# Kernel tuning notes

Hardware: AMD Instinct MI355X
Metric: run time of the kernel (lower is better)

## Reference

```python
import jax, jax.numpy as jnp
import numpy as np

DIM = 100
SAMPLE_DS = 0.5
MAX_S = int(DIM / SAMPLE_DS) + 1  # 201, matches torch sample_ds_arr
DIRECTIONS = ['x', 'x', 'y', 'y']  # constant in the original forward


def _polygon_area(poly):
    # poly: [bs, num_v, 2]; shoelace-style area identical to torch loop
    y_max = jnp.max(poly[:, :, 1], axis=-1)            # [bs]
    x0 = poly[:, :, 0]; y0 = poly[:, :, 1]
    x1 = jnp.roll(x0, -1, axis=1); y1 = jnp.roll(y0, -1, axis=1)
    s = jnp.sum((x1 - x0) * (y_max[:, None] - (y1 + y0) * 0.5), axis=1)
    return jnp.abs(s)


def _line_sum(mask_m, x0, x1, y0, y1, axis_x):
    # mask_m: [bs, DIM, DIM]; x0,x1,y0,y1: [bs, num_v]
    # Vectorized version of torch get_samples + interpolated_sum:
    # masked_select/dedup are replaced by boolean keep masks (samples along an
    # edge are monotone, so the valid set is a contiguous run and "previous
    # compacted sample" == "previous step").
    steps = jnp.arange(MAX_S, dtype=mask_m.dtype)      # [S]
    vx = x1 - x0 + 1e-6
    vy = y1 - y0 + 1e-6
    n = jnp.sqrt(vx * vx + vy * vy)
    vx = vx / n; vy = vy / n
    xs = x0[..., None] + steps * vx[..., None]         # [bs, nv, S]
    ys = y0[..., None] + steps * vy[..., None]
    xlo = jnp.minimum(x0, x1)[..., None]; xhi = jnp.maximum(x0, x1)[..., None]
    ylo = jnp.minimum(y0, y1)[..., None]; yhi = jnp.maximum(y0, y1)[..., None]
    seg = ((xs <= xhi + 1e-3) & (xs >= xlo - 1e-3) &
           (ys <= yhi + 1e-3) & (ys >= ylo - 1e-3))
    u = xs if axis_x else ys
    bound = (u <= DIM - 1) & (u >= 0.0)
    valid = seg & bound
    # dedup on floor(u) along sample axis (torch get_uniques)
    fu = jnp.floor(u)
    prev_valid = jnp.pad(valid[..., :-1], ((0, 0), (0, 0), (1, 0)))
    prev_fu = jnp.pad(fu[..., :-1], ((0, 0), (0, 0), (1, 0)))
    first = valid & ~prev_valid
    keep = valid & (first | (fu != prev_fu))
    # bilinear interpolation (torch interpolated_sum)
    X0f = jnp.floor(xs); Y0f = jnp.floor(ys)
    w00 = (X0f + 1 - xs) * (Y0f + 1 - ys)
    w01 = (X0f + 1 - xs) * (ys - Y0f)
    w10 = (xs - X0f) * (Y0f + 1 - ys)
    w11 = (xs - X0f) * (ys - Y0f)
    Xi0 = jnp.clip(X0f, 0, DIM - 1).astype(jnp.int32)
    Xi1 = jnp.clip(X0f + 1, 0, DIM - 1).astype(jnp.int32)
    Yi0 = jnp.clip(Y0f, 0, DIM - 1).astype(jnp.int32)
    Yi1 = jnp.clip(Y0f + 1, 0, DIM - 1).astype(jnp.int32)
    gather = jax.vmap(lambda m, yy, xx: m[yy, xx])      # over batch
    val = (w00 * gather(mask_m, Yi0, Xi0) + w01 * gather(mask_m, Yi1, Xi0) +
           w10 * gather(mask_m, Yi0, Xi1) + w11 * gather(mask_m, Yi1, Xi1))
    return jnp.sum(jnp.where(keep, val, 0.0), axis=-1)  # [bs, nv]


def _polygon_area_mask(poly, gt_mask):
    # poly: [bs, nv, 2], gt_mask: [bs, 4, DIM, DIM]
    x0 = poly[:, :, 0]; y0 = poly[:, :, 1]
    x1 = jnp.roll(x0, -1, axis=1); y1 = jnp.roll(y0, -1, axis=1)
    ret = jnp.zeros(poly.shape[0], dtype=poly.dtype)
    for m, d in enumerate(DIRECTIONS):
        ax = (d == 'x')
        sign = jnp.where((x1 > x0) if ax else (y1 > y0), 1.0, -1.0)
        sf = _line_sum(gt_mask[:, m], x0, x1, y0, y1, ax)
        sb = _line_sum(gt_mask[:, m], x1, x0, y1, y0, ax)
        s = jnp.sum(sign * (sf + sb) * 0.5, axis=1)
        ret = ret + jnp.abs(s)
    return ret / len(DIRECTIONS)


def setup_inputs() -> dict:
    key = jax.random.key(0)
    k1, k2, k3 = jax.random.split(key, 3)
    bs, nv = 512, 64
    poly = jax.random.uniform(k1, (bs, nv, 2), dtype=jnp.float32) * (DIM - 1)
    gt = jax.random.uniform(k2, (bs, nv, 2), dtype=jnp.float32) * (DIM - 1)
    gt_mask = jax.random.uniform(k3, (bs, 4, DIM, DIM), dtype=jnp.float32)
    return {"poly": poly, "gt": gt, "gt_mask": gt_mask}


def reference(poly, gt, gt_mask):
    pred_area = _polygon_area(poly)
    gt_area = _polygon_area(gt)
    int_area = _polygon_area_mask(poly, gt_mask)
    union_area = pred_area + gt_area - int_area
    return int_area / union_area
```

## Files before the change

### kernel.cpp

```cpp
#include <hip/hip_runtime.h>
#include <math.h>

#define DIM   100
#define NV    64
#define BS    512
#define MAXCH 1664
#define SMW   108
#define SMH   103

template<bool AX>
__device__ __forceinline__ float mainloop(
    const unsigned char* sm, const float4* prmA, const float4* prmB,
    const unsigned short* chunkTab, int totE, int tid) {
  const int grp = tid >> 5;
  const int sub = (tid >> 3) & 3;
  const int st  = tid & 7;
  const int base0 = grp * 16 + sub * 4;
  float acc = 0.0f;

  for (int i = 0; i * 128 < totE; ++i) {
    const ushort4 ent = *reinterpret_cast<const ushort4*>(
        &chunkTab[i * 128 + base0]);

    #define SAMPLE(e) {                                                    \
      const int c = (e) >> 4;                                              \
      const float kf = (float)((((e) & 15) << 3) | st);                    \
      const float4 p = prmA[c];                                            \
      const float4 q = prmB[c];                                            \
      const float vu = AX ? p.z : p.w;                                     \
      const float u0 = AX ? p.x : p.y;                                     \
      const float fu0 = floorf(u0);                                        \
      const float ck = fu0 + __builtin_copysignf(kf, vu);                  \
      const float te = ceilf(fmaf(kf, q.z, q.w));                          \
      const float u1 = __fadd_rn(__fmul_rn(te, vu), u0);                   \
      float t = (floorf(u1) == ck) ? te : (te + 1.0f);                     \
      t = fmaxf(t, 0.0f);                                                  \
      const float xs = __fadd_rn(__fmul_rn(t, p.z), p.x);                  \
      const float ys = __fadd_rn(__fmul_rn(t, p.w), p.y);                  \
      const float X0 = floorf(xs), Y0 = floorf(ys);                        \
      const float wx1 = xs - X0, wy1 = ys - Y0;                            \
      const float wx0 = 1.0f - wx1, wy0 = 1.0f - wy1;                      \
      const int ix = max(min((int)X0, 100), -1);                           \
      const int iy = max(min((int)Y0, 100), -1);                           \
      const int a = iy * SMW + ix;                                         \
      const float g00 = (float)sm[a + (SMW + 4)];                          \
      const float g10 = (float)sm[a + (SMW + 5)];                          \
      const float g01 = (float)sm[a + (2 * SMW + 4)];                      \
      const float g11 = (float)sm[a + (2 * SMW + 5)];                      \
      const float top = fmaf(wx1, g10, wx0 * g00);                         \
      const float bot = fmaf(wx1, g11, wx0 * g01);                         \
      const float val = fmaf(wy1, bot, wy0 * top);                         \
      const float w = (kf <= q.y) ? q.x : 0.0f;                            \
      acc = fmaf(w, val, acc);                                             \
    }
    SAMPLE(ent.x); SAMPLE(ent.y); SAMPLE(ent.z); SAMPLE(ent.w);
    #undef SAMPLE
  }
  return acc;
}

__global__ __launch_bounds__(256, 8) void diffiou_intersect(
    const float* __restrict__ poly, const float* __restrict__ gt_mask,
    float* __restrict__ ws) {
  __shared__ unsigned char sm[SMH * SMW];
  __shared__ float4 prmA[128];
  __shared__ float4 prmB[128];
  __shared__ unsigned short chunkTab[MAXCH];
  __shared__ int   wsum[2];
  __shared__ int   totalChunks;
  __shared__ float red[4];

  const int bid = blockIdx.x;
  const int b   = bid >> 2;
  const int m   = bid & 3;
  const bool ax = (m < 2);
  const int tid = threadIdx.x;

  const float*  src  = gt_mask + (size_t)(b * 4 + m) * (DIM * DIM);
  const float4* src4 = reinterpret_cast<const float4*>(src);

  float4 L0 = src4[tid];
  float4 L1 = src4[tid + 256];
  float4 L2 = src4[tid + 512];
  float4 L3 = src4[tid + 768];
  float4 L4 = src4[tid + 1024];

  #define CVTW(L, j) {                                                     \
    const int r_ = (j) / 25;                                               \
    const int g_ = (j) - r_ * 25;                                          \
    const unsigned int c0 = (unsigned int)__float2int_rn((L).x * 255.0f);  \
    const unsigned int c1 = (unsigned int)__float2int_rn((L).y * 255.0f);  \
    const unsigned int c2 = (unsigned int)__float2int_rn((L).z * 255.0f);  \
    const unsigned int c3 = (unsigned int)__float2int_rn((L).w * 255.0f);  \
    *reinterpret_cast<unsigned int*>(&sm[(r_ + 1) * SMW + 4 + 4 * g_]) =   \
        c0 | (c1 << 8) | (c2 << 16) | (c3 << 24);                          \
  }

  int ncv = 0;
  if (tid < 128) {
    const int e  = tid >> 1;
    const int fb = tid & 1;
    const float* pb = poly + (size_t)b * NV * 2;
    const float ex0 = pb[e * 2 + 0], ey0 = pb[e * 2 + 1];
    const int   en  = (e + 1) & (NV - 1);
    const float ex1 = pb[en * 2 + 0], ey1 = pb[en * 2 + 1];
    const float sign = (ax ? (ex1 > ex0) : (ey1 > ey0)) ? 1.0f : -1.0f;
    const float x0 = fb ? ex1 : ex0, y0 = fb ? ey1 : ey0;
    const float x1 = fb ? ex0 : ex1, y1 = fb ? ey0 : ey1;
    float vx = (x1 - x0) + 1e-6f;
    float vy = (y1 - y0) + 1e-6f;
    const float n = __fsqrt_rn(__fadd_rn(__fmul_rn(vx, vx), __fmul_rn(vy, vy)));
    vx = __fdiv_rn(vx, n);
    vy = __fdiv_rn(vy, n);
    float xlo = fminf(x0, x1) - 0.001f, xhi = fmaxf(x0, x1) + 0.001f;
    float ylo = fminf(y0, y1) - 0.001f, yhi = fmaxf(y0, y1) + 0.001f;
    if (ax) { xlo = fmaxf(xlo, 0.0f); xhi = fminf(xhi, (float)(DIM - 1)); }
    else    { ylo = fmaxf(ylo, 0.0f); yhi = fminf(yhi, (float)(DIM - 1)); }

    #define VALID_AT(tt, out_) {                                  \
      const float tf_ = (float)(tt);                              \
      const float xs_ = __fadd_rn(__fmul_rn(tf_, vx), x0);        \
      const float ys_ = __fadd_rn(__fmul_rn(tf_, vy), y0);        \
      out_ = (xs_ <= xhi) && (xs_ >= xlo) &&                      \
             (ys_ <= yhi) && (ys_ >= ylo);                        \
    }
    int T;
    bool v200; VALID_AT(200, v200);
    if (v200) { T = 200; }
    else {
      int lo = 0, hi = 200;
      #pragma unroll
      for (int it = 0; it < 8; ++it) {
        const int mid = (lo + hi) >> 1;
        bool vm; VALID_AT(mid, vm);
        if (vm) lo = mid; else hi = mid;
      }
      T = lo;
    }
    #undef VALID_AT

    const float vu  = ax ? vx : vy;
    const float u0  = ax ? x0 : y0;
    const float fu0 = floorf(u0);
    const float uT  = __fadd_rn(__fmul_rn((float)T, vu), u0);
    int K = abs((int)floorf(uT) - (int)fu0);
    K = min(K, 99);
    const float B = __fdiv_rn(1.0f, fabsf(vu));
    const float D = (vu > 0.0f) ? (fu0 - u0) : (u0 - fu0 - 1.0f);
    prmA[tid] = make_float4(x0, y0, vx, vy);
    prmB[tid] = make_float4(sign * (0.5f / 255.0f), (float)K,
                            B, fmaf(D, B, -0.005f));
    ncv = (K >> 3) + 1;
  }

  CVTW(L0, tid);
  CVTW(L1, tid + 256);
  CVTW(L2, tid + 512);
  CVTW(L3, tid + 768);
  CVTW(L4, tid + 1024);
  const int j5 = tid + 1280, j6 = tid + 1536, j7 = tid + 1792,
            j8 = tid + 2048, j9 = tid + 2304;
  L0 = src4[j5];
  L1 = src4[j6];
  L2 = src4[j7];
  L3 = src4[j8];
  L4 = (j9 < 2500) ? src4[j9] : make_float4(0.f, 0.f, 0.f, 0.f);

  int v = ncv;
  #pragma unroll
  for (int i = 1; i < 64; i <<= 1) {
    const int w = __shfl_up(v, i, 64);
    if ((tid & 63) >= i) v += w;
  }
  if (((tid & 63) == 63) && (tid < 128)) wsum[tid >> 6] = v;
  __syncthreads();
  if ((tid >= 64) && (tid < 128)) v += wsum[0];
  if (tid < 128) {
    const int start = v - ncv;
    for (int k = 0; k < ncv; ++k)
      chunkTab[start + k] = (unsigned short)((tid << 4) | k);
    if (tid == 127) totalChunks = v;
  }

  CVTW(L0, j5);
  CVTW(L1, j6);
  CVTW(L2, j7);
  CVTW(L3, j8);
  if (j9 < 2500) CVTW(L4, j9);
  if (tid < 75) {
    const int rr = tid / 25;
    const int g  = tid - rr * 25;
    const int srow = (rr == 0) ? 0 : (DIM - 1);
    const int drow = (rr == 0) ? 0 : (100 + rr);
    const float4 q = src4[srow * 25 + g];
    const unsigned int c0 = (unsigned int)__float2int_rn(q.x * 255.0f);
    const unsigned int c1 = (unsigned int)__float2int_rn(q.y * 255.0f);
    const unsigned int c2 = (unsigned int)__float2int_rn(q.z * 255.0f);
    const unsigned int c3 = (unsigned int)__float2int_rn(q.w * 255.0f);
    *reinterpret_cast<unsigned int*>(&sm[drow * SMW + 4 + 4 * g]) =
        c0 | (c1 << 8) | (c2 << 16) | (c3 << 24);
  }
  if (tid < SMH) {
    const int sr = min(max(tid - 1, 0), DIM - 1);
    const unsigned char e0 =
        (unsigned char)__float2int_rn(src[sr * DIM + 0] * 255.0f);
    const unsigned char e9 =
        (unsigned char)__float2int_rn(src[sr * DIM + DIM - 1] * 255.0f);
    sm[tid * SMW + 3] = e0;
    sm[tid * SMW + 104] = e9;
    sm[tid * SMW + 105] = e9;
  }
  #undef CVTW
  __syncthreads();

  const int totE = totalChunks;
  const int endE = (totE + 127) & ~127;
  if (totE + tid < endE) chunkTab[totE + tid] = 15;
  __syncthreads();

  const float acc = ax ? mainloop<true >(sm, prmA, prmB, chunkTab, totE, tid)
                       : mainloop<false>(sm, prmA, prmB, chunkTab, totE, tid);

  float a = acc;
  #pragma unroll
  for (int o = 32; o > 0; o >>= 1) a += __shfl_xor(a, o, 64);
  if ((tid & 63) == 0) red[tid >> 6] = a;
  __syncthreads();
  if (tid == 0) {
    const float s = red[0] + red[1] + red[2] + red[3];
    ws[bid] = fabsf(s);
  }
}

__device__ __forceinline__ float wave_area(const float* P, int b, int v) {
  const float x0 = P[(size_t)(b * NV + v) * 2 + 0];
  const float y0 = P[(size_t)(b * NV + v) * 2 + 1];
  const int vn = (v + 1) & (NV - 1);
  const float x1 = P[(size_t)(b * NV + vn) * 2 + 0];
  const float y1 = P[(size_t)(b * NV + vn) * 2 + 1];
  float ym = y0;
  #pragma unroll
  for (int o = 32; o > 0; o >>= 1) ym = fmaxf(ym, __shfl_xor(ym, o, 64));
  float term = (x1 - x0) * (ym - (y1 + y0) * 0.5f);
  #pragma unroll
  for (int o = 32; o > 0; o >>= 1) term += __shfl_xor(term, o, 64);
  return fabsf(term);
}

__global__ __launch_bounds__(64) void diffiou_finalize(
    const float* __restrict__ poly, const float* __restrict__ gt,
    const float* __restrict__ ws, float* __restrict__ out) {
  const int b = blockIdx.x;
  const int v = threadIdx.x;
  const float pa = wave_area(poly, b, v);
  const float ga = wave_area(gt, b, v);
  if (v == 0) {
    const float ia = 0.25f * (ws[b * 4 + 0] + ws[b * 4 + 1] +
                              ws[b * 4 + 2] + ws[b * 4 + 3]);
    out[b] = ia / (pa + ga - ia);
  }
}

extern "C" void kernel_launch(void* const* d_in, const int* in_sizes, int n_in,
                              void* d_out, int out_size, void* d_ws, size_t ws_size,
                              hipStream_t stream) {
  const float* poly    = (const float*)d_in[0];
  const float* gt      = (const float*)d_in[1];
  const float* gt_mask = (const float*)d_in[2];
  float* out = (float*)d_out;
  float* ws  = (float*)d_ws;

  hipLaunchKernelGGL(diffiou_intersect, dim3(BS * 4), dim3(256), 0, stream,
                     poly, gt_mask, ws);
  hipLaunchKernelGGL(diffiou_finalize, dim3(BS), dim3(64), 0, stream,
                     poly, gt, ws, out);
}
```

Measured before the change: 32.63 us.

## Store mask transposed in shared memory for x-direction blocks

```diff
diff --git a/kernel.cpp b/kernel.cpp
--- a/kernel.cpp
+++ b/kernel.cpp
@@ -39,18 +39,22 @@
       const float ys = __fadd_rn(__fmul_rn(t, p.w), p.y);                  \
       const float X0 = floorf(xs), Y0 = floorf(ys);                        \
       const float wx1 = xs - X0, wy1 = ys - Y0;                            \
-      const float wx0 = 1.0f - wx1, wy0 = 1.0f - wy1;                      \
       const int ix = max(min((int)X0, 100), -1);                           \
       const int iy = max(min((int)Y0, 100), -1);                           \
-      const int a = iy * SMW + ix;                                         \
-      const float g00 = (float)sm[a + (SMW + 4)];                          \
-      const float g10 = (float)sm[a + (SMW + 5)];                          \
-      const float g01 = (float)sm[a + (2 * SMW + 4)];                      \
-      const float g11 = (float)sm[a + (2 * SMW + 5)];                      \
-      const float top = fmaf(wx1, g10, wx0 * g00);                         \
-      const float bot = fmaf(wx1, g11, wx0 * g01);                         \
-      const float val = fmaf(wy1, bot, wy0 * top);                         \
-      const float w = (kf <= q.y) ? q.x : 0.0f;                            \
+      const int P = AX ? ix : iy;                    \
+      const int Q = AX ? iy : ix;                   \
+      const float wq1 = AX ? wy1 : wx1;             \
+      const float wp1 = AX ? wx1 : wy1;                                    \
+      const float wq0 = 1.0f - wq1, wp0 = 1.0f - wp1;                      \
+      const int a = P * SMW + Q;                                           \
+      const float g00 = (float)sm[a + (SMW + 4)];           \
+      const float gq1 = (float)sm[a + (SMW + 5)];           \
+      const float gp1 = (float)sm[a + (2 * SMW + 4)];       \
+      const float gpq = (float)sm[a + (2 * SMW + 5)];       \
+      const float top = fmaf(wq1, gq1, wq0 * g00);                         \
+      const float bot = fmaf(wq1, gpq, wq0 * gp1);                         \
+      const float val = fmaf(wp1, bot, wp0 * top);                         \
+      const float w = (kf <= q.y) ? q.x : 0.0f;                           \
       acc = fmaf(w, val, acc);                                             \
     }
     SAMPLE(ent.x); SAMPLE(ent.y); SAMPLE(ent.z); SAMPLE(ent.w);
@@ -79,12 +83,6 @@
   const float*  src  = gt_mask + (size_t)(b * 4 + m) * (DIM * DIM);
   const float4* src4 = reinterpret_cast<const float4*>(src);
 
-  float4 L0 = src4[tid];
-  float4 L1 = src4[tid + 256];
-  float4 L2 = src4[tid + 512];
-  float4 L3 = src4[tid + 768];
-  float4 L4 = src4[tid + 1024];
-
   #define CVTW(L, j) {                                                     \
     const int r_ = (j) / 25;                                               \
     const int g_ = (j) - r_ * 25;                                          \
@@ -94,6 +92,34 @@
     const unsigned int c3 = (unsigned int)__float2int_rn((L).w * 255.0f);  \
     *reinterpret_cast<unsigned int*>(&sm[(r_ + 1) * SMW + 4 + 4 * g_]) =   \
         c0 | (c1 << 8) | (c2 << 16) | (c3 << 24);                          \
+  }
+  #define LOADT(F, j) {                                                    \
+    const int g_ = (j) / 103;                                              \
+    const int r_ = (j) - g_ * 103;                                         \
+    const int xx = min(max(r_ - 1, 0), DIM - 1);                           \
+    (F).x = src[(4 * g_ + 0) * DIM + xx];                                  \
+    (F).y = src[(4 * g_ + 1) * DIM + xx];                                  \
+    (F).z = src[(4 * g_ + 2) * DIM + xx];                                  \
+    (F).w = src[(4 * g_ + 3) * DIM + xx];                                  \
+  }
+  #define CVTWT(F, j) {                                                    \
+    const int g_ = (j) / 103;                                              \
+    const int r_ = (j) - g_ * 103;                                         \
+    const unsigned int c0 = (unsigned int)__float2int_rn((F).x * 255.0f);  \
+    const unsigned int c1 = (unsigned int)__float2int_rn((F).y * 255.0f);  \
+    const unsigned int c2 = (unsigned int)__float2int_rn((F).z * 255.0f);  \
+    const unsigned int c3 = (unsigned int)__float2int_rn((F).w * 255.0f);  \
+    *reinterpret_cast<unsigned int*>(&sm[r_ * SMW + 4 + 4 * g_]) =         \
+        c0 | (c1 << 8) | (c2 << 16) | (c3 << 24);                          \
+  }
+
+  float4 L0, L1, L2, L3, L4;
+  if (ax) {
+    LOADT(L0, tid);        LOADT(L1, tid + 256);  LOADT(L2, tid + 512);
+    LOADT(L3, tid + 768);  LOADT(L4, tid + 1024);
+  } else {
+    L0 = src4[tid];        L1 = src4[tid + 256];  L2 = src4[tid + 512];
+    L3 = src4[tid + 768];  L4 = src4[tid + 1024];
   }
 
   int ncv = 0;
@@ -153,18 +179,19 @@
     ncv = (K >> 3) + 1;
   }
 
-  CVTW(L0, tid);
-  CVTW(L1, tid + 256);
-  CVTW(L2, tid + 512);
-  CVTW(L3, tid + 768);
-  CVTW(L4, tid + 1024);
   const int j5 = tid + 1280, j6 = tid + 1536, j7 = tid + 1792,
             j8 = tid + 2048, j9 = tid + 2304;
-  L0 = src4[j5];
-  L1 = src4[j6];
-  L2 = src4[j7];
-  L3 = src4[j8];
-  L4 = (j9 < 2500) ? src4[j9] : make_float4(0.f, 0.f, 0.f, 0.f);
+  if (ax) {
+    CVTWT(L0, tid);        CVTWT(L1, tid + 256);  CVTWT(L2, tid + 512);
+    CVTWT(L3, tid + 768);  CVTWT(L4, tid + 1024);
+    LOADT(L0, j5); LOADT(L1, j6); LOADT(L2, j7); LOADT(L3, j8);
+    if (j9 < 2575) LOADT(L4, j9);
+  } else {
+    CVTW(L0, tid);         CVTW(L1, tid + 256);   CVTW(L2, tid + 512);
+    CVTW(L3, tid + 768);   CVTW(L4, tid + 1024);
+    L0 = src4[j5]; L1 = src4[j6]; L2 = src4[j7]; L3 = src4[j8];
+    if (j9 < 2500) L4 = src4[j9];
+  }
 
   int v = ncv;
   #pragma unroll
@@ -182,35 +209,49 @@
     if (tid == 127) totalChunks = v;
   }
 
-  CVTW(L0, j5);
-  CVTW(L1, j6);
-  CVTW(L2, j7);
-  CVTW(L3, j8);
-  if (j9 < 2500) CVTW(L4, j9);
-  if (tid < 75) {
-    const int rr = tid / 25;
-    const int g  = tid - rr * 25;
-    const int srow = (rr == 0) ? 0 : (DIM - 1);
-    const int drow = (rr == 0) ? 0 : (100 + rr);
-    const float4 q = src4[srow * 25 + g];
-    const unsigned int c0 = (unsigned int)__float2int_rn(q.x * 255.0f);
-    const unsigned int c1 = (unsigned int)__float2int_rn(q.y * 255.0f);
-    const unsigned int c2 = (unsigned int)__float2int_rn(q.z * 255.0f);
-    const unsigned int c3 = (unsigned int)__float2int_rn(q.w * 255.0f);
-    *reinterpret_cast<unsigned int*>(&sm[drow * SMW + 4 + 4 * g]) =
-        c0 | (c1 << 8) | (c2 << 16) | (c3 << 24);
-  }
-  if (tid < SMH) {
-    const int sr = min(max(tid - 1, 0), DIM - 1);
-    const unsigned char e0 =
-        (unsigned char)__float2int_rn(src[sr * DIM + 0] * 255.0f);
-    const unsigned char e9 =
-        (unsigned char)__float2int_rn(src[sr * DIM + DIM - 1] * 255.0f);
-    sm[tid * SMW + 3] = e0;
-    sm[tid * SMW + 104] = e9;
-    sm[tid * SMW + 105] = e9;
+  if (ax) {
+    CVTWT(L0, j5); CVTWT(L1, j6); CVTWT(L2, j7); CVTWT(L3, j8);
+    if (j9 < 2575) CVTWT(L4, j9);
+    if (tid < SMH) {
+      const int xx = min(max(tid - 1, 0), DIM - 1);
+      const unsigned char e0 =
+          (unsigned char)__float2int_rn(src[0 * DIM + xx] * 255.0f);
+      const unsigned char e9 =
+          (unsigned char)__float2int_rn(src[(DIM - 1) * DIM + xx] * 255.0f);
+      sm[tid * SMW + 3] = e0;
+      sm[tid * SMW + 104] = e9;
+      sm[tid * SMW + 105] = e9;
+    }
+  } else {
+    CVTW(L0, j5); CVTW(L1, j6); CVTW(L2, j7); CVTW(L3, j8);
+    if (j9 < 2500) CVTW(L4, j9);
+    if (tid < 75) {
+      const int rr = tid / 25;
+      const int g  = tid - rr * 25;
+      const int srow = (rr == 0) ? 0 : (DIM - 1);
+      const int drow = (rr == 0) ? 0 : (100 + rr);
+      const float4 q = src4[srow * 25 + g];
+      const unsigned int c0 = (unsigned int)__float2int_rn(q.x * 255.0f);
+      const unsigned int c1 = (unsigned int)__float2int_rn(q.y * 255.0f);
+      const unsigned int c2 = (unsigned int)__float2int_rn(q.z * 255.0f);
+      const unsigned int c3 = (unsigned int)__float2int_rn(q.w * 255.0f);
+      *reinterpret_cast<unsigned int*>(&sm[drow * SMW + 4 + 4 * g]) =
+          c0 | (c1 << 8) | (c2 << 16) | (c3 << 24);
+    }
+    if (tid < SMH) {
+      const int sr = min(max(tid - 1, 0), DIM - 1);
+      const unsigned char e0 =
+          (unsigned char)__float2int_rn(src[sr * DIM + 0] * 255.0f);
+      const unsigned char e9 =
+          (unsigned char)__float2int_rn(src[sr * DIM + DIM - 1] * 255.0f);
+      sm[tid * SMW + 3] = e0;
+      sm[tid * SMW + 104] = e9;
+      sm[tid * SMW + 105] = e9;
+    }
   }
   #undef CVTW
+  #undef CVTWT
+  #undef LOADT
   __syncthreads();
 
   const int totE = totalChunks;
```

Result: faster. 30.83 us (-5.5%).
